# Kernel optimization log

Hardware: AMD Instinct MI355X
Metric: run time of the kernel (lower is better)

The kernel has to match this reference:

```python
import jax, jax.numpy as jnp
import numpy as np

N = 50000      # nodes
E = 800000     # edges
IN = 256       # in_dim
D = 64         # hidden_dim per head
H = 4          # heads
OUT = 40       # out_dim (classes)
SLOPE = 0.2    # leaky relu negative slope


def _gat_conv(h, src, dst, W, al, ar, heads, dh, res=None, act=False):
    """DGL-style GATConv. h:[N,Fin], W:[Fin,heads*dh], al/ar:[heads,dh]."""
    n = h.shape[0]
    feat = (h @ W).reshape(n, heads, dh)                 # [N,H,D]
    el = jnp.sum(feat * al, axis=-1)                     # [N,H]
    er = jnp.sum(feat * ar, axis=-1)                     # [N,H]
    e = jax.nn.leaky_relu(el[src] + er[dst], SLOPE)      # [E,H]
    # segment softmax over incoming edges of each dst node
    m = jax.ops.segment_max(e, dst, num_segments=n)      # [N,H]
    ex = jnp.exp(e - m[dst])                             # [E,H]
    s = jax.ops.segment_sum(ex, dst, num_segments=n)     # [N,H]
    alpha = ex / s[dst]                                  # [E,H]
    rst = jax.ops.segment_sum(alpha[:, :, None] * feat[src], dst, num_segments=n)  # [N,H,D]
    if res is not None:
        rst = rst + res
    if act:
        rst = jax.nn.elu(rst)
    return rst


def setup_inputs():
    key = jax.random.key(0)
    ks = jax.random.split(key, 16)
    def p(k, shape, fan_in):
        return (jax.random.normal(k, shape, jnp.float32) / np.sqrt(fan_in)).astype(jnp.float32)
    inputs = jax.random.normal(ks[0], (N, IN), jnp.float32)
    src = jax.random.randint(ks[1], (E,), 0, N, dtype=jnp.int32)
    dst = jax.random.randint(ks[2], (E,), 0, N, dtype=jnp.int32)
    return {
        "inputs": inputs, "src": src, "dst": dst,
        "W0": p(ks[3], (IN, H * D), IN), "al0": p(ks[4], (H, D), D), "ar0": p(ks[5], (H, D), D),
        "W1": p(ks[6], (H * D, H * D), H * D), "al1": p(ks[7], (H, D), D), "ar1": p(ks[8], (H, D), D),
        "Wo": p(ks[9], (H * D, H * OUT), H * D), "alo": p(ks[10], (H, OUT), OUT), "aro": p(ks[11], (H, OUT), OUT),
        "res_Wo": p(ks[12], (H * D, H * OUT), H * D),
        "fc_W": p(ks[13], (IN, D), IN),
    }


def reference(inputs, src, dst, W0, al0, ar0, W1, al1, ar1, Wo, alo, aro, res_Wo, fc_W):
    # layer 0: no residual, elu activation
    h = _gat_conv(inputs, src, dst, W0, al0, ar0, H, D, res=None, act=True)
    h = h.reshape(N, H * D)
    # layer 1: identity residual (in_feats == heads*out_feats), elu
    res1 = h.reshape(N, H, D)
    h = _gat_conv(h, src, dst, W1, al1, ar1, H, D, res=res1, act=True)
    h = h.reshape(N, H * D)
    # output layer: linear residual projection, no activation, mean over heads
    res_o = (h @ res_Wo).reshape(N, H, OUT)
    logits = _gat_conv(h, src, dst, Wo, alo, aro, H, OUT, res=res_o, act=False).mean(axis=1)
    seq_fts = inputs @ fc_W
    return (logits, h, seq_fts)
```

## Files before the change

kernel.cpp:

```cpp
#include <hip/hip_runtime.h>

typedef unsigned short u16;
typedef unsigned int u32;
typedef __attribute__((ext_vector_type(8))) short short8;
typedef __attribute__((ext_vector_type(4))) float f32x4;

#define NN 50000
#define EE 800000
#define EPAD (EE + 8*NN)

__device__ __forceinline__ float b2f(u16 u){ union{float f;u32 i;}x; x.i=((u32)u)<<16; return x.f; }
__device__ __forceinline__ u16 f2b(float f){ union{float f;u32 i;}x; x.f=f; u32 i=x.i; return (u16)((i + 0x7fffu + ((i>>16)&1u))>>16); }

__global__ void k_f2b4(const float* __restrict__ x, u16* __restrict__ y, int n4){
  int i = blockIdx.x*256 + threadIdx.x;
  if (i >= n4) return;
  float4 v = ((const float4*)x)[i];
  ushort4 o; o.x=f2b(v.x); o.y=f2b(v.y); o.z=f2b(v.z); o.w=f2b(v.w);
  ((ushort4*)y)[i]=o;
}

__global__ void k_wcvt(const float* __restrict__ W0, const float* __restrict__ W1, const float* __restrict__ fcW,
                       u16* __restrict__ W0b, u16* __restrict__ W1b, u16* __restrict__ fcb){
  int i = blockIdx.x*256 + threadIdx.x;
  const float* s; u16* d; int q;
  if (i < 16384){ s=W0; d=W0b; q=i; }
  else if (i < 32768){ s=W1; d=W1b; q=i-16384; }
  else if (i < 36864){ s=fcW; d=fcb; q=i-32768; }
  else return;
  float4 v = ((const float4*)s)[q];
  ushort4 o; o.x=f2b(v.x); o.y=f2b(v.y); o.z=f2b(v.z); o.w=f2b(v.w);
  ((ushort4*)d)[q]=o;
}

__global__ void k_catWo(const float* __restrict__ rWo, const float* __restrict__ Wo, u16* __restrict__ Bcat){
  int i = blockIdx.x*256 + threadIdx.x;
  if (i >= 256*320) return;
  int k = i/320, c = i%320;
  float v = (c < 160) ? rWo[k*160 + c] : Wo[k*160 + (c-160)];
  Bcat[i] = f2b(v);
}

__global__ void k_count(const int* __restrict__ dst, int* __restrict__ cnt){
  int i = blockIdx.x*256+threadIdx.x; if (i<EE) atomicAdd(&cnt[dst[i]],1);
}

__global__ void k_scan_blocks(const int* __restrict__ cnt, int* __restrict__ off, int* __restrict__ part, int n){
  __shared__ int ts[256];
  int t = threadIdx.x; int base = blockIdx.x*1024 + t*4;
  int c0 = (base+0<n)?((cnt[base+0]+7)&~7):0;
  int c1 = (base+1<n)?((cnt[base+1]+7)&~7):0;
  int c2 = (base+2<n)?((cnt[base+2]+7)&~7):0;
  int c3 = (base+3<n)?((cnt[base+3]+7)&~7):0;
  int s = c0+c1+c2+c3;
  ts[t]=s; __syncthreads();
  for (int d=1; d<256; d<<=1){ int v=(t>=d)?ts[t-d]:0; __syncthreads(); ts[t]+=v; __syncthreads(); }
  int ex = ts[t]-s;
  if (t==255) part[blockIdx.x]=ts[255];
  if (base+0<n) off[base+0]=ex; ex+=c0;
  if (base+1<n) off[base+1]=ex; ex+=c1;
  if (base+2<n) off[base+2]=ex; ex+=c2;
  if (base+3<n) off[base+3]=ex;
}

__global__ void k_scan_part(int* part, int nb){
  if (threadIdx.x==0 && blockIdx.x==0){ int run=0; for(int i=0;i<nb;++i){ int v=part[i]; part[i]=run; run+=v; } }
}

__global__ void k_addback(int* off, int* cur, const int* __restrict__ part, int n){
  int base = blockIdx.x*1024 + threadIdx.x*4; int p = part[blockIdx.x];
  #pragma unroll
  for (int j=0;j<4;++j) if (base+j<n){ int v = off[base+j]+p; off[base+j]=v; if (base+j<NN) cur[base+j]=v; }
}

__global__ void k_scatter(const int* __restrict__ src, const int* __restrict__ dst, int* __restrict__ cur,
                          int* __restrict__ srcs){
  int i = blockIdx.x*256+threadIdx.x; if (i>=EE) return;
  int d = dst[i]; int p = atomicAdd(&cur[d],1);
  srcs[p]=src[i];
}

template<int MODE>
__global__ __launch_bounds__(256) void k_gemm(const u16* __restrict__ A, const u16* __restrict__ B,
                                              void* __restrict__ C0, void* __restrict__ C1,
                                              int M, int N){
  __shared__ u16 Bt[64][266];
  const int tid = threadIdx.x;
  const int n0 = blockIdx.y * 64;
  const int row0 = blockIdx.x * 256;
  #pragma unroll
  for (int r=0; r<32; ++r){
    int lin = r*256 + tid;
    int kk = lin >> 5;
    int cp = (lin & 31) << 1;
    ushort2 v = *(const ushort2*)(B + (size_t)kk*N + n0 + cp);
    Bt[cp][kk] = v.x; Bt[cp+1][kk] = v.y;
  }
  __syncthreads();
  const int w = tid >> 6, l = tid & 63;
  const int lr = l & 15, lq = l >> 4;
  const int wrow = row0 + w*64;
  f32x4 acc[4][4];
  #pragma unroll
  for (int fr=0; fr<4; ++fr)
    #pragma unroll
    for (int j=0; j<4; ++j) acc[fr][j] = (f32x4)0.0f;
  #pragma unroll
  for (int k0 = 0; k0 < 256; k0 += 32){
    short8 a[4], b[4];
    #pragma unroll
    for (int fr=0; fr<4; ++fr){
      int r = wrow + fr*16 + lr; r = r < M ? r : M-1;
      a[fr] = *(const short8*)(A + (size_t)r*256 + k0 + lq*8);
    }
    #pragma unroll
    for (int j=0; j<4; ++j)
      b[j] = *(const short8*)(&Bt[j*16 + lr][k0 + lq*8]);
    #pragma unroll
    for (int fr=0; fr<4; ++fr)
      #pragma unroll
      for (int j=0; j<4; ++j)
        acc[fr][j] = __builtin_amdgcn_mfma_f32_16x16x32_bf16(a[fr], b[j], acc[fr][j], 0, 0, 0);
  }
  #pragma unroll
  for (int fr=0; fr<4; ++fr)
    #pragma unroll
    for (int j=0; j<4; ++j)
      #pragma unroll
      for (int q=0; q<4; ++q){
        int r = wrow + fr*16 + lq*4 + q;
        if (r < M){
          int c = n0 + j*16 + lr;
          float v = acc[fr][j][q];
          if constexpr (MODE == 0)      ((float*)C0)[(size_t)r*N + c] = v;
          else if constexpr (MODE == 1) ((u16*)C0)[(size_t)r*N + c] = f2b(v);
          else {
            if (c < 160) ((u16*)C0)[(size_t)r*160 + c]       = f2b(v);
            else         ((u16*)C1)[(size_t)r*160 + (c-160)] = f2b(v);
          }
        }
      }
}

__global__ void k_eler256(const u16* __restrict__ feat, const float* __restrict__ al, const float* __restrict__ ar,
                          float* __restrict__ el, float* __restrict__ er){
  int t = blockIdx.x*256 + threadIdx.x;
  int n = t >> 6, l = t & 63;
  if (n >= NN) return;
  float4 a4 = ((const float4*)al)[l];
  float4 r4 = ((const float4*)ar)[l];
  ushort4 f = *(const ushort4*)(feat + (size_t)n*256 + l*4);
  float f0=b2f(f.x), f1=b2f(f.y), f2=b2f(f.z), f3=b2f(f.w);
  float accl = f0*a4.x + f1*a4.y + f2*a4.z + f3*a4.w;
  float accr = f0*r4.x + f1*r4.y + f2*r4.z + f3*r4.w;
  #pragma unroll
  for (int m = 8; m >= 1; m >>= 1){ accl += __shfl_xor(accl, m, 64); accr += __shfl_xor(accr, m, 64); }
  int h = l >> 4;
  if ((l & 15) == 0){ el[n*4+h] = accl; er[n*4+h] = accr; }
}

__global__ void k_eler(const u16* __restrict__ feat, const float* __restrict__ al, const float* __restrict__ ar,
                       float* __restrict__ el, float* __restrict__ er, int Dh, int HD){
  int t = blockIdx.x*256 + threadIdx.x;
  int n = t >> 6; int l = t & 63;
  if (n >= NN) return;
  int h = l >> 4, s = l & 15;
  const u16* fr = feat + (size_t)n*HD + h*Dh;
  const float* alh = al + h*Dh; const float* arh = ar + h*Dh;
  float accl = 0.f, accr = 0.f;
  for (int d = s; d < Dh; d += 16){ float f = b2f(fr[d]); accl += f*alh[d]; accr += f*arh[d]; }
  #pragma unroll
  for (int m = 8; m >= 1; m >>= 1){ accl += __shfl_xor(accl, m, 64); accr += __shfl_xor(accr, m, 64); }
  if (s == 0){ el[n*4+h] = accl; er[n*4+h] = accr; }
}

__global__ void k_soft(const float* __restrict__ el, const float* __restrict__ er,
                       const int* __restrict__ srcs, const int* __restrict__ off, const int* __restrict__ cnt,
                       float* __restrict__ es, float* __restrict__ recs){
  int t = blockIdx.x*256 + threadIdx.x;
  int n = t >> 4; if (n >= NN) return;
  int g = t & 15;
  int o0 = off[n], o1p = off[n+1];
  int deg = cnt[n];
  int oend = o0 + deg;
  float4 e4 = ((const float4*)er)[n];
  float4 m; m.x=m.y=m.z=m.w=-1e30f;
  for (int c = o0 + g; c < oend; c += 16){
    float4 a = ((const float4*)el)[srcs[c]];
    float4 v;
    v.x=a.x+e4.x; v.x = v.x>=0.f?v.x:0.2f*v.x;
    v.y=a.y+e4.y; v.y = v.y>=0.f?v.y:0.2f*v.y;
    v.z=a.z+e4.z; v.z = v.z>=0.f?v.z:0.2f*v.z;
    v.w=a.w+e4.w; v.w = v.w>=0.f?v.w:0.2f*v.w;
    ((float4*)es)[c]=v;
    m.x=fmaxf(m.x,v.x); m.y=fmaxf(m.y,v.y); m.z=fmaxf(m.z,v.z); m.w=fmaxf(m.w,v.w);
  }
  { int cp = oend + g; if (cp < o1p){ float4 z; z.x=z.y=z.z=z.w=0.f; ((float4*)es)[cp]=z; } }
  #pragma unroll
  for (int msk = 8; msk >= 1; msk >>= 1){
    m.x=fmaxf(m.x,__shfl_xor(m.x,msk,64)); m.y=fmaxf(m.y,__shfl_xor(m.y,msk,64));
    m.z=fmaxf(m.z,__shfl_xor(m.z,msk,64)); m.w=fmaxf(m.w,__shfl_xor(m.w,msk,64));
  }
  float4 s; s.x=s.y=s.z=s.w=0.f;
  for (int c = o0 + g; c < oend; c += 16){
    float4 v = ((const float4*)es)[c];
    v.x=__expf(v.x-m.x); v.y=__expf(v.y-m.y); v.z=__expf(v.z-m.z); v.w=__expf(v.w-m.w);
    ((float4*)es)[c]=v; s.x+=v.x; s.y+=v.y; s.z+=v.z; s.w+=v.w;
  }
  #pragma unroll
  for (int msk = 8; msk >= 1; msk >>= 1){
    s.x+=__shfl_xor(s.x,msk,64); s.y+=__shfl_xor(s.y,msk,64);
    s.z+=__shfl_xor(s.z,msk,64); s.w+=__shfl_xor(s.w,msk,64);
  }
  if (g == 0){
    float4 r;
    r.x = s.x>0.f ? 1.f/s.x : 0.f;
    r.y = s.y>0.f ? 1.f/s.y : 0.f;
    r.z = s.z>0.f ? 1.f/s.z : 0.f;
    r.w = s.w>0.f ? 1.f/s.w : 0.f;
    ((float4*)recs)[n] = r;
  }
}

template<bool RES>
__global__ __launch_bounds__(256) void k_agg64(const u16* __restrict__ feat, const float* __restrict__ es,
    const float* __restrict__ recs, const int* __restrict__ off, const int* __restrict__ srcs,
    const u16* __restrict__ resid, float* __restrict__ outf, u16* __restrict__ outb){
  const int l = threadIdx.x & 63, w = threadIdx.x >> 6;
  const int n = blockIdx.x*4 + w;
  const int o0 = off[n], o1p = off[n+1];
  const int lh = l & 31;
  const int half = l >> 5;
  const int h = lh >> 3;
  float a0=0.f,a1=0.f,a2=0.f,a3=0.f,a4=0.f,a5=0.f,a6=0.f,a7=0.f;
  for (int i = o0; i < o1p; i += 8){
    #pragma unroll
    for (int u=0; u<4; ++u){
      int e = i + u*2 + half;
      int sv = srcs[e];
      float al = es[(size_t)e*4 + h];
      short8 f = *(const short8*)(feat + (size_t)sv*256 + lh*8);
      a0 += al*b2f((u16)f[0]); a1 += al*b2f((u16)f[1]);
      a2 += al*b2f((u16)f[2]); a3 += al*b2f((u16)f[3]);
      a4 += al*b2f((u16)f[4]); a5 += al*b2f((u16)f[5]);
      a6 += al*b2f((u16)f[6]); a7 += al*b2f((u16)f[7]);
    }
  }
  a0 += __shfl_xor(a0,32,64); a1 += __shfl_xor(a1,32,64);
  a2 += __shfl_xor(a2,32,64); a3 += __shfl_xor(a3,32,64);
  a4 += __shfl_xor(a4,32,64); a5 += __shfl_xor(a5,32,64);
  a6 += __shfl_xor(a6,32,64); a7 += __shfl_xor(a7,32,64);
  if (half == 0){
    float rc = recs[n*4+h];
    float v[8] = {a0*rc,a1*rc,a2*rc,a3*rc,a4*rc,a5*rc,a6*rc,a7*rc};
    if (RES){
      short8 r8 = *(const short8*)(resid + (size_t)n*256 + lh*8);
      #pragma unroll
      for (int j=0;j<8;++j) v[j] += b2f((u16)r8[j]);
    }
    #pragma unroll
    for (int j=0;j<8;++j) v[j] = v[j] > 0.f ? v[j] : expm1f(v[j]);
    if (outf){
      float4 q0; q0.x=v[0]; q0.y=v[1]; q0.z=v[2]; q0.w=v[3];
      float4 q1; q1.x=v[4]; q1.y=v[5]; q1.z=v[6]; q1.w=v[7];
      *(float4*)(outf + (size_t)n*256 + lh*8)     = q0;
      *(float4*)(outf + (size_t)n*256 + lh*8 + 4) = q1;
    }
    short8 ob;
    #pragma unroll
    for (int j=0;j<8;++j) ob[j] = (short)f2b(v[j]);
    *(short8*)(outb + (size_t)n*256 + lh*8) = ob;
  }
}

__global__ __launch_bounds__(256) void k_agg_out(const u16* __restrict__ feat, const float* __restrict__ es,
    const float* __restrict__ recs, const int* __restrict__ off, const int* __restrict__ srcs,
    const u16* __restrict__ reso, float* __restrict__ logits){
  __shared__ float red[4][8][20][8];
  __shared__ float fin[4][160];
  const int l = threadIdx.x & 63, w = threadIdx.x >> 6;
  const int n = blockIdx.x*4 + w;
  const int o0 = off[n], o1p = off[n+1];
  const int s0 = l/20,        q0 = l%20;
  const int s1 = (64+l)/20,   q1 = (64+l)%20;
  const int s2 = (128+l)/20,  q2 = (128+l)%20;
  const int h0 = q0/5, h1 = q1/5, h2 = q2/5;
  float acc0[8], acc1[8], acc2[8];
  #pragma unroll
  for (int j=0;j<8;++j){ acc0[j]=0.f; acc1[j]=0.f; acc2[j]=0.f; }
  for (int i0 = o0; i0 < o1p; i0 += 8){
    {
      int e = i0 + s0; int sv = srcs[e]; float al = es[(size_t)e*4 + h0];
      short8 f = *(const short8*)(feat + (size_t)sv*160 + q0*8);
      #pragma unroll
      for (int j=0;j<8;++j) acc0[j] += al*b2f((u16)f[j]);
    }
    {
      int e = i0 + s1; int sv = srcs[e]; float al = es[(size_t)e*4 + h1];
      short8 f = *(const short8*)(feat + (size_t)sv*160 + q1*8);
      #pragma unroll
      for (int j=0;j<8;++j) acc1[j] += al*b2f((u16)f[j]);
    }
    if (l < 32){
      int e = i0 + s2; int sv = srcs[e]; float al = es[(size_t)e*4 + h2];
      short8 f = *(const short8*)(feat + (size_t)sv*160 + q2*8);
      #pragma unroll
      for (int j=0;j<8;++j) acc2[j] += al*b2f((u16)f[j]);
    }
  }
  #pragma unroll
  for (int j=0;j<8;++j) red[w][s0][q0][j] = acc0[j];
  #pragma unroll
  for (int j=0;j<8;++j) red[w][s1][q1][j] = acc1[j];
  if (l < 32){
    #pragma unroll
    for (int j=0;j<8;++j) red[w][s2][q2][j] = acc2[j];
  }
  __syncthreads();
  if (l < 20){
    const int q = l;
    float rc = recs[n*4 + q/5];
    short8 rr = *(const short8*)(reso + (size_t)n*160 + q*8);
    #pragma unroll
    for (int j=0;j<8;++j){
      float v = red[w][0][q][j];
      #pragma unroll
      for (int s=1;s<8;++s) v += red[w][s][q][j];
      fin[w][q*8+j] = v*rc + b2f((u16)rr[j]);
    }
  }
  __syncthreads();
  if (l < 40) logits[(size_t)n*40 + l] = 0.25f*(fin[w][l]+fin[w][l+40]+fin[w][l+80]+fin[w][l+120]);
}

extern "C" void kernel_launch(void* const* d_in, const int* in_sizes, int n_in,
                              void* d_out, int out_size, void* d_ws, size_t ws_size,
                              hipStream_t stream){
  const float* inputs = (const float*)d_in[0];
  const int*   src    = (const int*)d_in[1];
  const int*   dst    = (const int*)d_in[2];
  const float* W0  = (const float*)d_in[3];
  const float* al0 = (const float*)d_in[4];
  const float* ar0 = (const float*)d_in[5];
  const float* W1  = (const float*)d_in[6];
  const float* al1 = (const float*)d_in[7];
  const float* ar1 = (const float*)d_in[8];
  const float* Wo  = (const float*)d_in[9];
  const float* alo = (const float*)d_in[10];
  const float* aro = (const float*)d_in[11];
  const float* rWo = (const float*)d_in[12];
  const float* fcW = (const float*)d_in[13];

  float* out = (float*)d_out;
  float* out_logits = out;
  float* out_h      = out + 2000000;
  float* out_seq    = out + 14800000;

  char* ws = (char*)d_ws;
  size_t o = 0;
  auto alc = [&](size_t bytes){ size_t r = o; o += (bytes + 255) & ~(size_t)255; return r; };
  size_t oXb   = alc((size_t)NN*256*2);
  size_t oFA   = alc((size_t)NN*256*2);
  size_t oFB   = alc((size_t)NN*256*2);
  size_t oEs   = alc((size_t)EPAD*4*4);
  size_t oSrcs = alc((size_t)EPAD*4);
  size_t oOff  = alc((size_t)(NN+1)*4);
  size_t oCnt  = alc((size_t)(NN+1)*4);
  size_t oCur  = alc((size_t)NN*4);
  size_t oPart = alc(64*4);
  size_t oEl   = alc((size_t)NN*4*4);
  size_t oEr   = alc((size_t)NN*4*4);
  size_t oRecs = alc((size_t)NN*4*4);
  size_t oReso = alc((size_t)NN*160*2);
  size_t oW0b  = alc(256*256*2);
  size_t oW1b  = alc(256*256*2);
  size_t oWcat = alc(256*320*2);
  size_t oFcb  = alc(256*64*2);
  if (ws_size < o) return;

  u16* Xb   = (u16*)(ws + oXb);
  u16* fA   = (u16*)(ws + oFA);
  u16* fB   = (u16*)(ws + oFB);
  float* es = (float*)(ws + oEs);
  int* srcs = (int*)(ws + oSrcs);
  int* off  = (int*)(ws + oOff);
  int* cnt  = (int*)(ws + oCnt);
  int* cur  = (int*)(ws + oCur);
  int* part = (int*)(ws + oPart);
  float* el = (float*)(ws + oEl);
  float* er = (float*)(ws + oEr);
  float* recs = (float*)(ws + oRecs);
  u16* reso = (u16*)(ws + oReso);
  u16* W0b  = (u16*)(ws + oW0b);
  u16* W1b  = (u16*)(ws + oW1b);
  u16* Wcat = (u16*)(ws + oWcat);
  u16* fcb  = (u16*)(ws + oFcb);

  k_f2b4<<<(NN*256/4 + 255)/256, 256, 0, stream>>>(inputs, Xb, NN*256/4);
  k_wcvt<<<(36864 + 255)/256, 256, 0, stream>>>(W0, W1, fcW, W0b, W1b, fcb);
  k_catWo<<<(256*320 + 255)/256, 256, 0, stream>>>(rWo, Wo, Wcat);

  hipMemsetAsync(cnt, 0, (size_t)(NN+1)*4, stream);
  hipMemsetAsync(srcs, 0, (size_t)EPAD*4, stream);
  k_count<<<(EE+255)/256, 256, 0, stream>>>(dst, cnt);
  const int NP1 = NN+1, NB = (NP1 + 1023)/1024;
  k_scan_blocks<<<NB, 256, 0, stream>>>(cnt, off, part, NP1);
  k_scan_part<<<1, 64, 0, stream>>>(part, NB);
  k_addback<<<NB, 256, 0, stream>>>(off, cur, part, NP1);
  k_scatter<<<(EE+255)/256, 256, 0, stream>>>(src, dst, cur, srcs);

  dim3 gN256((NN+255)/256, 4), gN320((NN+255)/256, 5), gN64((NN+255)/256, 1);

  k_gemm<0><<<gN64, 256, 0, stream>>>(Xb, fcb, out_seq, nullptr, NN, 64);

  k_gemm<1><<<gN256, 256, 0, stream>>>(Xb, W0b, fA, nullptr, NN, 256);
  k_eler256<<<(NN*64 + 255)/256, 256, 0, stream>>>(fA, al0, ar0, el, er);
  k_soft<<<(NN*16 + 255)/256, 256, 0, stream>>>(el, er, srcs, off, cnt, es, recs);
  k_agg64<false><<<NN/4, 256, 0, stream>>>(fA, es, recs, off, srcs, nullptr, nullptr, fB);

  k_gemm<1><<<gN256, 256, 0, stream>>>(fB, W1b, fA, nullptr, NN, 256);
  k_eler256<<<(NN*64 + 255)/256, 256, 0, stream>>>(fA, al1, ar1, el, er);
  k_soft<<<(NN*16 + 255)/256, 256, 0, stream>>>(el, er, srcs, off, cnt, es, recs);
  k_agg64<true><<<NN/4, 256, 0, stream>>>(fA, es, recs, off, srcs, fB, out_h, fB);

  k_gemm<2><<<gN320, 256, 0, stream>>>(fB, Wcat, reso, fA, NN, 320);
  k_eler<<<(NN*64 + 255)/256, 256, 0, stream>>>(fA, alo, aro, el, er, 40, 160);
  k_soft<<<(NN*16 + 255)/256, 256, 0, stream>>>(el, er, srcs, off, cnt, es, recs);
  k_agg_out<<<NN/4, 256, 0, stream>>>(fA, es, recs, off, srcs, reso, out_logits);
}
```

Before: 507.0 us.

## Stage GEMM A/B tiles in swizzled LDS via direct global-to-LDS loads

Weights are pre-transposed to N-major bf16 so that both A (128-row tile) and B tiles can be copied straight into LDS with global_load_lds and an XOR swizzle. MFMA operands are then read from LDS instead of global memory, and a 2x2 wave layout replaces the earlier 256-row by 64-column tiling. This is meant to cut redundant global A reads and the scalar transposing B stores. The aggregation loop also gains a 16-edge unrolled main body to raise memory-level parallelism. The 128KB LDS footprint limits occupancy, and the last row tile reads past NN into neighbouring workspace, though those stores are masked.

```diff
diff --git a/kernel.cpp b/kernel.cpp
--- a/kernel.cpp
+++ b/kernel.cpp
@@ -20,25 +20,19 @@
   ((ushort4*)y)[i]=o;
 }
 
-__global__ void k_wcvt(const float* __restrict__ W0, const float* __restrict__ W1, const float* __restrict__ fcW,
-                       u16* __restrict__ W0b, u16* __restrict__ W1b, u16* __restrict__ fcb){
+__global__ void k_wtr(const float* __restrict__ W, u16* __restrict__ Wt, int N){
   int i = blockIdx.x*256 + threadIdx.x;
-  const float* s; u16* d; int q;
-  if (i < 16384){ s=W0; d=W0b; q=i; }
-  else if (i < 32768){ s=W1; d=W1b; q=i-16384; }
-  else if (i < 36864){ s=fcW; d=fcb; q=i-32768; }
-  else return;
-  float4 v = ((const float4*)s)[q];
-  ushort4 o; o.x=f2b(v.x); o.y=f2b(v.y); o.z=f2b(v.z); o.w=f2b(v.w);
-  ((ushort4*)d)[q]=o;
-}
-
-__global__ void k_catWo(const float* __restrict__ rWo, const float* __restrict__ Wo, u16* __restrict__ Bcat){
+  if (i >= 256*N) return;
+  int k = i / N, n = i % N;
+  Wt[(size_t)n*256 + k] = f2b(W[i]);
+}
+
+__global__ void k_catWoT(const float* __restrict__ rWo, const float* __restrict__ Wo, u16* __restrict__ Bct){
   int i = blockIdx.x*256 + threadIdx.x;
   if (i >= 256*320) return;
   int k = i/320, c = i%320;
   float v = (c < 160) ? rWo[k*160 + c] : Wo[k*160 + (c-160)];
-  Bcat[i] = f2b(v);
+  Bct[(size_t)c*256 + k] = f2b(v);
 }
 
 __global__ void k_count(const int* __restrict__ dst, int* __restrict__ cnt){
@@ -80,63 +74,80 @@
   srcs[p]=src[i];
 }
 
-template<int MODE>
-__global__ __launch_bounds__(256) void k_gemm(const u16* __restrict__ A, const u16* __restrict__ B,
-                                              void* __restrict__ C0, void* __restrict__ C1,
-                                              int M, int N){
-  __shared__ u16 Bt[64][266];
+template<int BN, int MODE>
+__global__ __launch_bounds__(256) void k_gemm2(const u16* __restrict__ A, const u16* __restrict__ Bt,
+                                               void* __restrict__ C0, void* __restrict__ C1,
+                                               int M, int ldC){
+  __shared__ u16 lds[(128+BN)*256];
+  u16* As = lds;
+  u16* Bs = lds + 128*256;
   const int tid = threadIdx.x;
-  const int n0 = blockIdx.y * 64;
-  const int row0 = blockIdx.x * 256;
-  #pragma unroll
-  for (int r=0; r<32; ++r){
-    int lin = r*256 + tid;
-    int kk = lin >> 5;
-    int cp = (lin & 31) << 1;
-    ushort2 v = *(const ushort2*)(B + (size_t)kk*N + n0 + cp);
-    Bt[cp][kk] = v.x; Bt[cp+1][kk] = v.y;
+  const int row0 = blockIdx.x * 128;
+  const int n0   = blockIdx.y * BN;
+  #pragma unroll
+  for (int it=0; it<16; ++it){
+    int slot = it*256 + tid;
+    int r = slot >> 5, s = slot & 31;
+    int gs = s ^ (r & 7);
+    const u16* gp = A + (size_t)(row0 + r)*256 + (gs<<3);
+    u16* lp = As + (size_t)(it*256 + (tid & ~63))*8;
+    __builtin_amdgcn_global_load_lds((const void*)gp, (void*)lp, 16, 0, 0);
+  }
+  #pragma unroll
+  for (int it=0; it<BN/8; ++it){
+    int slot = it*256 + tid;
+    int r = slot >> 5, s = slot & 31;
+    int gs = s ^ (r & 7);
+    const u16* gp = Bt + (size_t)(n0 + r)*256 + (gs<<3);
+    u16* lp = Bs + (size_t)(it*256 + (tid & ~63))*8;
+    __builtin_amdgcn_global_load_lds((const void*)gp, (void*)lp, 16, 0, 0);
   }
   __syncthreads();
-  const int w = tid >> 6, l = tid & 63;
+  const int wave = tid >> 6, l = tid & 63;
+  const int wm = wave >> 1, wn = wave & 1;
   const int lr = l & 15, lq = l >> 4;
-  const int wrow = row0 + w*64;
+  const int NR = BN/32;
   f32x4 acc[4][4];
   #pragma unroll
-  for (int fr=0; fr<4; ++fr)
-    #pragma unroll
-    for (int j=0; j<4; ++j) acc[fr][j] = (f32x4)0.0f;
-  #pragma unroll
-  for (int k0 = 0; k0 < 256; k0 += 32){
+  for (int mr=0;mr<4;++mr)
+    #pragma unroll
+    for (int nr=0;nr<NR;++nr) acc[mr][nr]=(f32x4)0.0f;
+  #pragma unroll
+  for (int kk=0; kk<8; ++kk){
     short8 a[4], b[4];
     #pragma unroll
-    for (int fr=0; fr<4; ++fr){
-      int r = wrow + fr*16 + lr; r = r < M ? r : M-1;
-      a[fr] = *(const short8*)(A + (size_t)r*256 + k0 + lq*8);
-    }
-    #pragma unroll
-    for (int j=0; j<4; ++j)
-      b[j] = *(const short8*)(&Bt[j*16 + lr][k0 + lq*8]);
-    #pragma unroll
-    for (int fr=0; fr<4; ++fr)
-      #pragma unroll
-      for (int j=0; j<4; ++j)
-        acc[fr][j] = __builtin_amdgcn_mfma_f32_16x16x32_bf16(a[fr], b[j], acc[fr][j], 0, 0, 0);
-  }
-  #pragma unroll
-  for (int fr=0; fr<4; ++fr)
-    #pragma unroll
-    for (int j=0; j<4; ++j)
-      #pragma unroll
-      for (int q=0; q<4; ++q){
-        int r = wrow + fr*16 + lq*4 + q;
+    for (int mr=0;mr<4;++mr){
+      int rloc = wm*64 + mr*16 + lr;
+      int byo = rloc*512 + ((kk*64 + lq*16) ^ ((rloc&7)<<4));
+      a[mr] = *(const short8*)((const char*)As + byo);
+    }
+    #pragma unroll
+    for (int nr=0;nr<NR;++nr){
+      int cloc = wn*(BN/2) + nr*16 + lr;
+      int byo = cloc*512 + ((kk*64 + lq*16) ^ ((cloc&7)<<4));
+      b[nr] = *(const short8*)((const char*)Bs + byo);
+    }
+    #pragma unroll
+    for (int mr=0;mr<4;++mr)
+      #pragma unroll
+      for (int nr=0;nr<NR;++nr)
+        acc[mr][nr] = __builtin_amdgcn_mfma_f32_16x16x32_bf16(a[mr], b[nr], acc[mr][nr], 0, 0, 0);
+  }
+  #pragma unroll
+  for (int mr=0;mr<4;++mr)
+    #pragma unroll
+    for (int nr=0;nr<NR;++nr)
+      #pragma unroll
+      for (int q=0;q<4;++q){
+        int r = row0 + wm*64 + mr*16 + lq*4 + q;
         if (r < M){
-          int c = n0 + j*16 + lr;
-          float v = acc[fr][j][q];
-          if constexpr (MODE == 0)      ((float*)C0)[(size_t)r*N + c] = v;
-          else if constexpr (MODE == 1) ((u16*)C0)[(size_t)r*N + c] = f2b(v);
+          int c = n0 + wn*(BN/2) + nr*16 + lr;
+          float v = acc[mr][nr][q];
+          if constexpr (MODE == 0)      ((float*)C0)[(size_t)r*ldC + c] = v;
+          else if constexpr (MODE == 1) ((u16*)C0)[(size_t)r*ldC + c] = f2b(v);
           else {
-            if (c < 160) ((u16*)C0)[(size_t)r*160 + c]       = f2b(v);
-            else         ((u16*)C1)[(size_t)r*160 + (c-160)] = f2b(v);
+            if (c < 160)      ((u16*)C0)[(size_t)r*160 + c]       = f2b(v);
+            else if (c < 320) ((u16*)C1)[(size_t)r*160 + (c-160)] = f2b(v);
           }
         }
       }
@@ -233,7 +244,21 @@
   const int half = l >> 5;
   const int h = lh >> 3;
   float a0=0.f,a1=0.f,a2=0.f,a3=0.f,a4=0.f,a5=0.f,a6=0.f,a7=0.f;
-  for (int i = o0; i < o1p; i += 8){
+  int i = o0;
+  for (; i + 16 <= o1p; i += 16){
+    #pragma unroll
+    for (int u=0; u<8; ++u){
+      int e = i + u*2 + half;
+      int sv = srcs[e];
+      float al = es[(size_t)e*4 + h];
+      short8 f = *(const short8*)(feat + (size_t)sv*256 + lh*8);
+      a0 += al*b2f((u16)f[0]); a1 += al*b2f((u16)f[1]);
+      a2 += al*b2f((u16)f[2]); a3 += al*b2f((u16)f[3]);
+      a4 += al*b2f((u16)f[4]); a5 += al*b2f((u16)f[5]);
+      a6 += al*b2f((u16)f[6]); a7 += al*b2f((u16)f[7]);
+    }
+  }
+  if (i < o1p){
     #pragma unroll
     for (int u=0; u<4; ++u){
       int e = i + u*2 + half;
@@ -372,10 +397,10 @@
   size_t oEr   = alc((size_t)NN*4*4);
   size_t oRecs = alc((size_t)NN*4*4);
   size_t oReso = alc((size_t)NN*160*2);
-  size_t oW0b  = alc(256*256*2);
-  size_t oW1b  = alc(256*256*2);
-  size_t oWcat = alc(256*320*2);
-  size_t oFcb  = alc(256*64*2);
+  size_t oW0t  = alc(256*256*2);
+  size_t oW1t  = alc(256*256*2);
+  size_t oWct  = alc((size_t)384*256*2);
+  size_t oFct  = alc((size_t)128*256*2);
   if (ws_size < o) return;
 
   u16* Xb   = (u16*)(ws + oXb);
@@ -391,14 +416,16 @@
   float* er = (float*)(ws + oEr);
   float* recs = (float*)(ws + oRecs);
   u16* reso = (u16*)(ws + oReso);
-  u16* W0b  = (u16*)(ws + oW0b);
-  u16* W1b  = (u16*)(ws + oW1b);
-  u16* Wcat = (u16*)(ws + oWcat);
-  u16* fcb  = (u16*)(ws + oFcb);
+  u16* W0t  = (u16*)(ws + oW0t);
+  u16* W1t  = (u16*)(ws + oW1t);
+  u16* Wct  = (u16*)(ws + oWct);
+  u16* fct  = (u16*)(ws + oFct);
 
   k_f2b4<<<(NN*256/4 + 255)/256, 256, 0, stream>>>(inputs, Xb, NN*256/4);
-  k_wcvt<<<(36864 + 255)/256, 256, 0, stream>>>(W0, W1, fcW, W0b, W1b, fcb);
-  k_catWo<<<(256*320 + 255)/256, 256, 0, stream>>>(rWo, Wo, Wcat);
+  k_wtr<<<(256*256 + 255)/256, 256, 0, stream>>>(W0, W0t, 256);
+  k_wtr<<<(256*256 + 255)/256, 256, 0, stream>>>(W1, W1t, 256);
+  k_wtr<<<(256*64 + 255)/256, 256, 0, stream>>>(fcW, fct, 64);
+  k_catWoT<<<(256*320 + 255)/256, 256, 0, stream>>>(rWo, Wo, Wct);
 
   hipMemsetAsync(cnt, 0, (size_t)(NN+1)*4, stream);
   hipMemsetAsync(srcs, 0, (size_t)EPAD*4, stream);
@@ -409,21 +436,22 @@
   k_addback<<<NB, 256, 0, stream>>>(off, cur, part, NP1);
   k_scatter<<<(EE+255)/256, 256, 0, stream>>>(src, dst, cur, srcs);
 
-  dim3 gN256((NN+255)/256, 4), gN320((NN+255)/256, 5), gN64((NN+255)/256, 1);
-
-  k_gemm<0><<<gN64, 256, 0, stream>>>(Xb, fcb, out_seq, nullptr, NN, 64);
-
-  k_gemm<1><<<gN256, 256, 0, stream>>>(Xb, W0b, fA, nullptr, NN, 256);
+  const int GX = (NN + 127)/128;
+  dim3 g256(GX, 2), g320(GX, 3), g64(GX, 1);
+
+  k_gemm2<64,0><<<g64, 256, 0, stream>>>(Xb, fct, out_seq, nullptr, NN, 64);
+
+  k_gemm2<128,1><<<g256, 256, 0, stream>>>(Xb, W0t, fA, nullptr, NN, 256);
   k_eler256<<<(NN*64 + 255)/256, 256, 0, stream>>>(fA, al0, ar0, el, er);
   k_soft<<<(NN*16 + 255)/256, 256, 0, stream>>>(el, er, srcs, off, cnt, es, recs);
   k_agg64<false><<<NN/4, 256, 0, stream>>>(fA, es, recs, off, srcs, nullptr, nullptr, fB);
 
-  k_gemm<1><<<gN256, 256, 0, stream>>>(fB, W1b, fA, nullptr, NN, 256);
+  k_gemm2<128,1><<<g256, 256, 0, stream>>>(fB, W1t, fA, nullptr, NN, 256);
   k_eler256<<<(NN*64 + 255)/256, 256, 0, stream>>>(fA, al1, ar1, el, er);
   k_soft<<<(NN*16 + 255)/256, 256, 0, stream>>>(el, er, srcs, off, cnt, es, recs);
   k_agg64<true><<<NN/4, 256, 0, stream>>>(fA, es, recs, off, srcs, fB, out_h, fB);
 
-  k_gemm<2><<<gN320, 256, 0, stream>>>(fB, Wcat, reso, fA, NN, 320);
+  k_gemm2<128,2><<<g320, 256, 0, stream>>>(fB, Wct, reso, fA, NN, 320);
   k_eler<<<(NN*64 + 255)/256, 256, 0, stream>>>(fA, alo, aro, el, er, 40, 160);
   k_soft<<<(NN*16 + 255)/256, 256, 0, stream>>>(el, er, srcs, off, cnt, es, recs);
   k_agg_out<<<NN/4, 256, 0, stream>>>(fA, es, recs, off, srcs, reso, out_logits);
```

After: 489.7 us. 3.4% less time.
